# Kernel optimization log

Measured on AMD Instinct MI355X. Metric: run time of the kernel, lower is better.

## Reference

```python
import jax, jax.numpy as jnp
from jax import lax
import numpy as np

K = 3          # kernelsize
RX = RY = 3.0  # dilated_rates * kernelsize
BN_EPS = 1e-3  # keras BatchNormalization default


def setup_inputs() -> dict:
    key = jax.random.key(0)
    k1, k2, k3 = jax.random.split(key, 3)
    B, H, W, C, F = 8, 128, 128, 64, 64
    return {
        "fmap": jax.random.normal(k1, (B, H, W, C), jnp.float32),
        "y2": jax.random.normal(k2, (B, H, W, 8), jnp.float32),
        "conv_w": jax.random.normal(k3, (K, K, C, F), jnp.float32) * np.sqrt(2.0 / (K * K * C)),
        "gamma": jnp.ones((F,), jnp.float32),
        "beta": jnp.zeros((F,), jnp.float32),
        "moving_mean": jnp.zeros((F,), jnp.float32),
        "moving_var": jnp.ones((F,), jnp.float32),
    }


def reference(fmap, y2, conv_w, gamma, beta, moving_mean, moving_var):
    B, H, W, C = fmap.shape
    HW = H * W
    N = HW * K * K

    xs = jnp.clip(jnp.flip(jnp.sort(y2[..., 0:4], axis=-1), -1)[..., 0:2], 1.0, W - 1)  # [B,H,W,2]
    ys = jnp.clip(jnp.flip(jnp.sort(y2[..., 4:8], axis=-1), -1)[..., 0:2], 1.0, H - 1)
    w = jnp.sum(xs, axis=-1, keepdims=True)  # [B,H,W,1]
    h = jnp.sum(ys, axis=-1, keepdims=True)

    # base pixel grids flattened as in the TF code: row[i*W+j]=i, column[i*W+j]=j
    row = jnp.repeat(jnp.arange(H, dtype=jnp.float32), W).reshape(HW, 1)
    column = jnp.tile(jnp.arange(W, dtype=jnp.float32), H).reshape(HW, 1)

    wf = (w / RX).reshape(B, HW, 1)
    w0 = (w * 1e-10).reshape(B, HW, 1)
    x_samp = jnp.concatenate([column - 1.0 - wf, column + w0, column + 1.0 + wf], axis=-1)  # [B,HW,3]
    x_samp = jnp.tile(x_samp.reshape(-1, H, W, 1), (1, 1, 1, K))  # [3B,H,W,3] (same layout as TF)

    hf = (h / RY).reshape(B, HW, 1)
    h0 = (h * 1e-10).reshape(B, HW, 1)
    y_samp = jnp.concatenate([row - 1.0 - hf, row + h0, row + 1.0 + hf], axis=-1)
    y_samp = jnp.tile(y_samp.reshape(-1, H, W, 1), (1, 1, 1, K))  # [3B,H,W,3]

    x_left = jnp.clip(jnp.floor(x_samp), 0.0, W - 1)
    x_right = jnp.clip(jnp.ceil(x_samp), 0.0, W - 1)
    y_top = jnp.clip(jnp.floor(y_samp), 0.0, H - 1)
    y_bottom = jnp.clip(jnp.ceil(y_samp), 0.0, H - 1)

    def flat(a):  # -> [B, N, 1] (broadcast over C replaces TF's tile)
        return a.reshape(-1, N)[:, :, None]

    xr_x = flat(x_right - x_samp)
    xl_x = flat(x_samp - x_left)
    yt_y = flat(y_samp - y_top)
    yb_y = flat(y_bottom - y_samp)

    idx_lt = (y_top * W + x_left).reshape(-1, N).astype(jnp.int32)
    idx_rt = (y_top * W + x_right).reshape(-1, N).astype(jnp.int32)
    idx_lb = (y_bottom * W + x_left).reshape(-1, N).astype(jnp.int32)
    idx_rb = (y_bottom * W + x_right).reshape(-1, N).astype(jnp.int32)

    fmap2 = fmap.reshape(B, HW, C)
    gather = lambda idx: jnp.take_along_axis(fmap2, idx[:, :, None], axis=1)  # [B,N,C]

    f_lt, f_rt = gather(idx_lt), gather(idx_rt)
    f_lb, f_rb = gather(idx_lb), gather(idx_rb)

    f = (xr_x * f_lt + xl_x * f_lb) * yb_y + (xr_x * f_rt + xl_x * f_rb) * yt_y  # [B,N,C]
    f = f.reshape(-1, H * K, W * K, C)  # [B, 3H, 3W, C]

    out = lax.conv_general_dilated(
        f, conv_w, window_strides=(K, K), padding="VALID",
        dimension_numbers=("NHWC", "HWIO", "NHWC"))  # [B,H,W,F]

    out = (out - moving_mean) * (gamma / jnp.sqrt(moving_var + BN_EPS)) + beta
    return jax.nn.relu(out)
```

## Files before the change

kernel.cpp:

```cpp
#include <hip/hip_runtime.h>

typedef __bf16 bf16x8 __attribute__((ext_vector_type(8)));
typedef float f32x4 __attribute__((ext_vector_type(4)));

__device__ __forceinline__ unsigned short f2bf(float f) {
  __bf16 h = (__bf16)f;
  return __builtin_bit_cast(unsigned short, h);
}

__global__ __launch_bounds__(256) void prep_kernel(
    const float* __restrict__ conv_w, const float* __restrict__ gamma,
    const float* __restrict__ beta, const float* __restrict__ mean,
    const float* __restrict__ var, unsigned short* __restrict__ wsB,
    float* __restrict__ bias) {
  int idx = blockIdx.x * 256 + threadIdx.x;
  if (idx >= 12288) return;
  int di    = idx >> 12;
  int r     = idx & 4095;
  int jblk  = r >> 10;
  int r2    = r & 1023;
  int kstep = r2 >> 9;
  int r3    = r2 & 511;
  int lane  = r3 >> 3;
  int i     = r3 & 7;
  int c   = kstep * 32 + 4 * (lane >> 4) + (i & 3) + 16 * (i >> 2);
  int fch = jblk * 16 + (lane & 15);
  float s = gamma[fch] * rsqrtf(var[fch] + 1e-3f);
  float v = conv_w[((di * 3 + 0) * 64 + c) * 64 + fch]
          + conv_w[((di * 3 + 1) * 64 + c) * 64 + fch]
          + conv_w[((di * 3 + 2) * 64 + c) * 64 + fch];
  wsB[idx] = f2bf(v * s);
  if (idx < 64) bias[idx] = beta[idx] - mean[idx] * (gamma[idx] * rsqrtf(var[idx] + 1e-3f));
}

__global__ __launch_bounds__(256, 4) void main_kernel(
    const float* __restrict__ fmap, const float* __restrict__ y2,
    const uint4* __restrict__ wsBq, const float* __restrict__ biasg,
    float* __restrict__ out) {
  __shared__ int   s_idx[4][384];
  __shared__ float s_wt[4][384];
  __shared__ uint2 fsA[16][64][2];

  const int t    = threadIdx.x;
  const int lane = t & 63;
  const int wave = t >> 6;
  const int b  = blockIdx.x & 7;
  const int oi = blockIdx.x >> 3;
  const float* fmapb = fmap + (size_t)b * (128 * 128 * 64);

  for (int u = t; u < 384; u += 256) {
    int j = u / 3;
    int a = u - j * 3;
    const float4* yp = reinterpret_cast<const float4*>(
        y2 + ((size_t)(b * 128 + oi) * 128 + j) * 8);
    float4 xv = yp[0];
    float4 yv = yp[1];

    float hi01 = fmaxf(xv.x, xv.y), lo01 = fminf(xv.x, xv.y);
    float hi23 = fmaxf(xv.z, xv.w), lo23 = fminf(xv.z, xv.w);
    float top1 = fmaxf(hi01, hi23);
    float top2 = fmaxf(fminf(hi01, hi23), (hi01 >= hi23) ? lo01 : lo23);
    float w = fminf(fmaxf(top1, 1.f), 127.f) + fminf(fmaxf(top2, 1.f), 127.f);

    hi01 = fmaxf(yv.x, yv.y); lo01 = fminf(yv.x, yv.y);
    hi23 = fmaxf(yv.z, yv.w); lo23 = fminf(yv.z, yv.w);
    top1 = fmaxf(hi01, hi23);
    top2 = fmaxf(fminf(hi01, hi23), (hi01 >= hi23) ? lo01 : lo23);
    float h = fminf(fmaxf(top1, 1.f), 127.f) + fminf(fmaxf(top2, 1.f), 127.f);

    float x, yy;
    if (a == 0)      { x = ((float)j - 1.0f) - w / 3.0f;  yy = ((float)oi - 1.0f) - h / 3.0f; }
    else if (a == 1) { x = (float)j + w * 1e-10f;         yy = (float)oi + h * 1e-10f; }
    else             { x = ((float)j + 1.0f) + w / 3.0f;  yy = ((float)oi + 1.0f) + h / 3.0f; }

    float xl = fminf(fmaxf(floorf(x), 0.f), 127.f);
    float xr = fminf(fmaxf(ceilf(x),  0.f), 127.f);
    float yt = fminf(fmaxf(floorf(yy), 0.f), 127.f);
    float yb = fminf(fmaxf(ceilf(yy),  0.f), 127.f);
    int ixl = (int)xl, ixr = (int)xr, iyt = (int)yt, iyb = (int)yb;
    s_idx[0][u] = (iyt * 128 + ixl) * 64;
    s_idx[1][u] = (iyt * 128 + ixr) * 64;
    s_idx[2][u] = (iyb * 128 + ixl) * 64;
    s_idx[3][u] = (iyb * 128 + ixr) * 64;
    s_wt[0][u] = xr - x;
    s_wt[1][u] = x - xl;
    s_wt[2][u] = yy - yt;
    s_wt[3][u] = yb - yy;
  }
  __syncthreads();

  float bias4[4];
  #pragma unroll
  for (int j = 0; j < 4; ++j) bias4[j] = biasg[j * 16 + (lane & 15)];

  f32x4 acc[2][4];
  #pragma unroll
  for (int p = 0; p < 2; ++p)
    #pragma unroll
    for (int j = 0; j < 4; ++j)
      acc[p][j] = (f32x4){0.f, 0.f, 0.f, 0.f};

  for (int di = 0; di < 3; ++di) {
    bf16x8 Bf[8];
    #pragma unroll
    for (int jk = 0; jk < 8; ++jk)
      Bf[jk] = __builtin_bit_cast(bf16x8, wsBq[(di * 8 + jk) * 64 + lane]);

    #pragma unroll 2
    for (int r = 0; r < 8; ++r) {
      int task = t + 256 * r;
      int up = task >> 4;
      int cg = task & 15;
      int c0 = cg * 4;
      int u  = di * 128 + up;
      int i0 = s_idx[0][u], i1 = s_idx[1][u], i2 = s_idx[2][u], i3 = s_idx[3][u];
      float4 lt = *reinterpret_cast<const float4*>(fmapb + i0 + c0);
      float4 rt = *reinterpret_cast<const float4*>(fmapb + i1 + c0);
      float4 lb = *reinterpret_cast<const float4*>(fmapb + i2 + c0);
      float4 rb = *reinterpret_cast<const float4*>(fmapb + i3 + c0);
      float xr_x = s_wt[0][u], xl_x = s_wt[1][u];
      float yt_y = s_wt[2][u], yb_y = s_wt[3][u];
      float v0 = (xr_x * lt.x + xl_x * lb.x) * yb_y + (xr_x * rt.x + xl_x * rb.x) * yt_y;
      float v1 = (xr_x * lt.y + xl_x * lb.y) * yb_y + (xr_x * rt.y + xl_x * rb.y) * yt_y;
      float v2 = (xr_x * lt.z + xl_x * lb.z) * yb_y + (xr_x * rt.z + xl_x * rb.z) * yt_y;
      float v3 = (xr_x * lt.w + xl_x * lb.w) * yb_y + (xr_x * rt.w + xl_x * rb.w) * yt_y;
      uint2 q;
      q.x = (unsigned)f2bf(v0) | ((unsigned)f2bf(v1) << 16);
      q.y = (unsigned)f2bf(v2) | ((unsigned)f2bf(v3) << 16);
      int kstep = cg >> 3, g = cg & 3, h = (cg >> 2) & 1;
      fsA[(up >> 4) * 2 + kstep][(up & 15) + 16 * g][h] = q;
    }
    __syncthreads();

    #pragma unroll
    for (int kstep = 0; kstep < 2; ++kstep) {
      #pragma unroll
      for (int p = 0; p < 2; ++p) {
        int pxblk = wave * 2 + p;
        bf16x8 a = __builtin_bit_cast(bf16x8,
            *reinterpret_cast<const uint4*>(&fsA[pxblk * 2 + kstep][lane][0]));
        #pragma unroll
        for (int j = 0; j < 4; ++j)
          acc[p][j] = __builtin_amdgcn_mfma_f32_16x16x32_bf16(a, Bf[j * 2 + kstep],
                                                              acc[p][j], 0, 0, 0);
      }
    }
    __syncthreads();
  }

  float* outb = out + ((size_t)(b * 128 + oi) * 128) * 64;
  #pragma unroll
  for (int p = 0; p < 2; ++p) {
    int pxB = (wave * 2 + p) * 16 + (lane >> 4) * 4;
    #pragma unroll
    for (int j = 0; j < 4; ++j) {
      int fch = j * 16 + (lane & 15);
      #pragma unroll
      for (int reg = 0; reg < 4; ++reg) {
        float v = acc[p][j][reg] + bias4[j];
        outb[(size_t)(pxB + reg) * 64 + fch] = fmaxf(v, 0.f);
      }
    }
  }
}

extern "C" void kernel_launch(void* const* d_in, const int* in_sizes, int n_in,
                              void* d_out, int out_size, void* d_ws, size_t ws_size,
                              hipStream_t stream) {
  const float* fmap   = (const float*)d_in[0];
  const float* y2     = (const float*)d_in[1];
  const float* conv_w = (const float*)d_in[2];
  const float* gamma  = (const float*)d_in[3];
  const float* beta   = (const float*)d_in[4];
  const float* mean   = (const float*)d_in[5];
  const float* var    = (const float*)d_in[6];
  float* outp = (float*)d_out;

  unsigned short* wsB = (unsigned short*)d_ws;
  float* bias = (float*)((char*)d_ws + 24576);

  prep_kernel<<<48, 256, 0, stream>>>(conv_w, gamma, beta, mean, var, wsB, bias);
  main_kernel<<<1024, 256, 0, stream>>>(fmap, y2, (const uint4*)d_ws, bias, outp);
}
```

Before: 34.10 us.

## Skip gathers for zero-weight samples, swizzle LDS tile, fold bias into accumulator

During setup, each sample position is classified by whether its bilinear weights can contribute. Contributing positions are compacted into a per-tap list in shared memory using LDS atomics, and the rest are written as zeros without any fmap gather or arithmetic. The centre tap's float offsets usually round to exact integers, so most of its gathers can be skipped. The fsA tile is also XOR-swizzled to reduce LDS bank conflicts, and the bias now initialises the accumulators. In exchange this adds atomics, an extra barrier and a divergent branch, and it assumes zero weights always give zero output, which does not hold if the gathered values contain inf or NaN.

After: 30.86 us. -9.5%, faster.

```diff
diff --git a/kernel.cpp b/kernel.cpp
--- a/kernel.cpp
+++ b/kernel.cpp
@@ -40,6 +40,8 @@
   __shared__ int   s_idx[4][384];
   __shared__ float s_wt[4][384];
   __shared__ uint2 fsA[16][64][2];
+  __shared__ unsigned char lst[3][128];
+  __shared__ int cnt[3], zc[3];
 
   const int t    = threadIdx.x;
   const int lane = t & 63;
@@ -47,6 +49,10 @@
   const int b  = blockIdx.x & 7;
   const int oi = blockIdx.x >> 3;
   const float* fmapb = fmap + (size_t)b * (128 * 128 * 64);
+
+  if (t < 3) cnt[t] = 0;
+  else if (t < 6) zc[t - 3] = 0;
+  __syncthreads();
 
   for (int u = t; u < 384; u += 256) {
     int j = u / 3;
@@ -82,10 +88,17 @@
     s_idx[1][u] = (iyt * 128 + ixr) * 64;
     s_idx[2][u] = (iyb * 128 + ixl) * 64;
     s_idx[3][u] = (iyb * 128 + ixr) * 64;
-    s_wt[0][u] = xr - x;
-    s_wt[1][u] = x - xl;
-    s_wt[2][u] = yy - yt;
-    s_wt[3][u] = yb - yy;
+    float xr_x = xr - x, xl_x = x - xl, yt_y = yy - yt, yb_y = yb - yy;
+    s_wt[0][u] = xr_x;
+    s_wt[1][u] = xl_x;
+    s_wt[2][u] = yt_y;
+    s_wt[3][u] = yb_y;
+
+    bool need = ((xr_x != 0.f) || (xl_x != 0.f)) && ((yb_y != 0.f) || (yt_y != 0.f));
+    int di = u >> 7;
+    int up = u & 127;
+    int pos = need ? atomicAdd(&cnt[di], 1) : (127 - atomicAdd(&zc[di], 1));
+    lst[di][pos] = (unsigned char)up;
   }
   __syncthreads();
 
@@ -98,47 +111,56 @@
   for (int p = 0; p < 2; ++p)
     #pragma unroll
     for (int j = 0; j < 4; ++j)
-      acc[p][j] = (f32x4){0.f, 0.f, 0.f, 0.f};
+      acc[p][j] = (f32x4){bias4[j], bias4[j], bias4[j], bias4[j]};
 
   for (int di = 0; di < 3; ++di) {
     bf16x8 Bf[8];
     #pragma unroll
     for (int jk = 0; jk < 8; ++jk)
       Bf[jk] = __builtin_bit_cast(bf16x8, wsBq[(di * 8 + jk) * 64 + lane]);
+
+    const int nzc = cnt[di];
 
     #pragma unroll 2
     for (int r = 0; r < 8; ++r) {
       int task = t + 256 * r;
-      int up = task >> 4;
-      int cg = task & 15;
-      int c0 = cg * 4;
-      int u  = di * 128 + up;
-      int i0 = s_idx[0][u], i1 = s_idx[1][u], i2 = s_idx[2][u], i3 = s_idx[3][u];
-      float4 lt = *reinterpret_cast<const float4*>(fmapb + i0 + c0);
-      float4 rt = *reinterpret_cast<const float4*>(fmapb + i1 + c0);
-      float4 lb = *reinterpret_cast<const float4*>(fmapb + i2 + c0);
-      float4 rb = *reinterpret_cast<const float4*>(fmapb + i3 + c0);
-      float xr_x = s_wt[0][u], xl_x = s_wt[1][u];
-      float yt_y = s_wt[2][u], yb_y = s_wt[3][u];
-      float v0 = (xr_x * lt.x + xl_x * lb.x) * yb_y + (xr_x * rt.x + xl_x * rb.x) * yt_y;
-      float v1 = (xr_x * lt.y + xl_x * lb.y) * yb_y + (xr_x * rt.y + xl_x * rb.y) * yt_y;
-      float v2 = (xr_x * lt.z + xl_x * lb.z) * yb_y + (xr_x * rt.z + xl_x * rb.z) * yt_y;
-      float v3 = (xr_x * lt.w + xl_x * lb.w) * yb_y + (xr_x * rt.w + xl_x * rb.w) * yt_y;
-      uint2 q;
-      q.x = (unsigned)f2bf(v0) | ((unsigned)f2bf(v1) << 16);
-      q.y = (unsigned)f2bf(v2) | ((unsigned)f2bf(v3) << 16);
-      int kstep = cg >> 3, g = cg & 3, h = (cg >> 2) & 1;
-      fsA[(up >> 4) * 2 + kstep][(up & 15) + 16 * g][h] = q;
+      int gidx = task >> 4;
+      int cg   = task & 15;
+      int up   = lst[di][gidx];
+      int kstep = cg >> 3, g = cg & 3, hh = (cg >> 2) & 1;
+      int sA  = (up >> 4) * 2 + kstep;
+      int lA  = (up & 15) + 16 * g;
+      int lsw = lA ^ (2 * g);
+      uint2 q = make_uint2(0u, 0u);
+      if (gidx < nzc) {
+        int c0 = cg * 4;
+        int u  = di * 128 + up;
+        int i0 = s_idx[0][u], i1 = s_idx[1][u], i2 = s_idx[2][u], i3 = s_idx[3][u];
+        float4 lt = *reinterpret_cast<const float4*>(fmapb + i0 + c0);
+        float4 rt = *reinterpret_cast<const float4*>(fmapb + i1 + c0);
+        float4 lb = *reinterpret_cast<const float4*>(fmapb + i2 + c0);
+        float4 rb = *reinterpret_cast<const float4*>(fmapb + i3 + c0);
+        float xr_x = s_wt[0][u], xl_x = s_wt[1][u];
+        float yt_y = s_wt[2][u], yb_y = s_wt[3][u];
+        float v0 = (xr_x * lt.x + xl_x * lb.x) * yb_y + (xr_x * rt.x + xl_x * rb.x) * yt_y;
+        float v1 = (xr_x * lt.y + xl_x * lb.y) * yb_y + (xr_x * rt.y + xl_x * rb.y) * yt_y;
+        float v2 = (xr_x * lt.z + xl_x * lb.z) * yb_y + (xr_x * rt.z + xl_x * rb.z) * yt_y;
+        float v3 = (xr_x * lt.w + xl_x * lb.w) * yb_y + (xr_x * rt.w + xl_x * rb.w) * yt_y;
+        q.x = (unsigned)f2bf(v0) | ((unsigned)f2bf(v1) << 16);
+        q.y = (unsigned)f2bf(v2) | ((unsigned)f2bf(v3) << 16);
+      }
+      fsA[sA][lsw][hh] = q;
     }
     __syncthreads();
 
+    const int lsr = lane ^ (2 * (lane >> 4));
     #pragma unroll
     for (int kstep = 0; kstep < 2; ++kstep) {
       #pragma unroll
       for (int p = 0; p < 2; ++p) {
         int pxblk = wave * 2 + p;
         bf16x8 a = __builtin_bit_cast(bf16x8,
-            *reinterpret_cast<const uint4*>(&fsA[pxblk * 2 + kstep][lane][0]));
+            *reinterpret_cast<const uint4*>(&fsA[pxblk * 2 + kstep][lsr][0]));
         #pragma unroll
         for (int j = 0; j < 4; ++j)
           acc[p][j] = __builtin_amdgcn_mfma_f32_16x16x32_bf16(a, Bf[j * 2 + kstep],
@@ -157,8 +179,7 @@
       int fch = j * 16 + (lane & 15);
       #pragma unroll
       for (int reg = 0; reg < 4; ++reg) {
-        float v = acc[p][j][reg] + bias4[j];
-        outb[(size_t)(pxB + reg) * 64 + fch] = fmaxf(v, 0.f);
+        outb[(size_t)(pxB + reg) * 64 + fch] = fmaxf(acc[p][j][reg], 0.f);
       }
     }
   }
```

## Gather bilinear samples directly into MFMA A-fragments, drop LDS staging

Applied to the files above, without the earlier changes.

Each lane now loads and interpolates the fmap samples for exactly the A-fragment elements it feeds to the MFMA, instead of writing bf16 samples to shared memory and reading them back. This removes the fsA buffer and two block barriers per di iteration. It also skips the gathers when all bilinear weights are zero, and folds the bias into the accumulator initialisation. In exchange, each lane issues more scattered 16-byte loads, and the loads from one lane are split across two 16-float channel groups rather than staying contiguous.

Result: slower. 48.78 us (+43.0%).

```diff
diff --git a/kernel.cpp b/kernel.cpp
--- a/kernel.cpp
+++ b/kernel.cpp
@@ -39,7 +39,6 @@
     float* __restrict__ out) {
   __shared__ int   s_idx[4][384];
   __shared__ float s_wt[4][384];
-  __shared__ uint2 fsA[16][64][2];
 
   const int t    = threadIdx.x;
   const int lane = t & 63;
@@ -89,16 +88,19 @@
   }
   __syncthreads();
 
+  const int px15 = lane & 15;
+  const int cgrp = lane >> 4;
+
   float bias4[4];
   #pragma unroll
-  for (int j = 0; j < 4; ++j) bias4[j] = biasg[j * 16 + (lane & 15)];
+  for (int j = 0; j < 4; ++j) bias4[j] = biasg[j * 16 + px15];
 
   f32x4 acc[2][4];
   #pragma unroll
   for (int p = 0; p < 2; ++p)
     #pragma unroll
     for (int j = 0; j < 4; ++j)
-      acc[p][j] = (f32x4){0.f, 0.f, 0.f, 0.f};
+      acc[p][j] = (f32x4){bias4[j], bias4[j], bias4[j], bias4[j]};
 
   for (int di = 0; di < 3; ++di) {
     bf16x8 Bf[8];
@@ -106,46 +108,50 @@
     for (int jk = 0; jk < 8; ++jk)
       Bf[jk] = __builtin_bit_cast(bf16x8, wsBq[(di * 8 + jk) * 64 + lane]);
 
-    #pragma unroll 2
-    for (int r = 0; r < 8; ++r) {
-      int task = t + 256 * r;
-      int up = task >> 4;
-      int cg = task & 15;
-      int c0 = cg * 4;
-      int u  = di * 128 + up;
-      int i0 = s_idx[0][u], i1 = s_idx[1][u], i2 = s_idx[2][u], i3 = s_idx[3][u];
-      float4 lt = *reinterpret_cast<const float4*>(fmapb + i0 + c0);
-      float4 rt = *reinterpret_cast<const float4*>(fmapb + i1 + c0);
-      float4 lb = *reinterpret_cast<const float4*>(fmapb + i2 + c0);
-      float4 rb = *reinterpret_cast<const float4*>(fmapb + i3 + c0);
-      float xr_x = s_wt[0][u], xl_x = s_wt[1][u];
-      float yt_y = s_wt[2][u], yb_y = s_wt[3][u];
-      float v0 = (xr_x * lt.x + xl_x * lb.x) * yb_y + (xr_x * rt.x + xl_x * rb.x) * yt_y;
-      float v1 = (xr_x * lt.y + xl_x * lb.y) * yb_y + (xr_x * rt.y + xl_x * rb.y) * yt_y;
-      float v2 = (xr_x * lt.z + xl_x * lb.z) * yb_y + (xr_x * rt.z + xl_x * rb.z) * yt_y;
-      float v3 = (xr_x * lt.w + xl_x * lb.w) * yb_y + (xr_x * rt.w + xl_x * rb.w) * yt_y;
-      uint2 q;
-      q.x = (unsigned)f2bf(v0) | ((unsigned)f2bf(v1) << 16);
-      q.y = (unsigned)f2bf(v2) | ((unsigned)f2bf(v3) << 16);
-      int kstep = cg >> 3, g = cg & 3, h = (cg >> 2) & 1;
-      fsA[(up >> 4) * 2 + kstep][(up & 15) + 16 * g][h] = q;
-    }
-    __syncthreads();
+    #pragma unroll
+    for (int p = 0; p < 2; ++p) {
+      const int up = (wave * 2 + p) * 16 + px15;
+      const int u  = di * 128 + up;
+      const int i0 = s_idx[0][u], i1 = s_idx[1][u];
+      const int i2 = s_idx[2][u], i3 = s_idx[3][u];
+      const float xr_x = s_wt[0][u], xl_x = s_wt[1][u];
+      const float yt_y = s_wt[2][u], yb_y = s_wt[3][u];
+      const bool need = ((xr_x != 0.f) || (xl_x != 0.f)) &&
+                        ((yb_y != 0.f) || (yt_y != 0.f));
 
-    #pragma unroll
-    for (int kstep = 0; kstep < 2; ++kstep) {
       #pragma unroll
-      for (int p = 0; p < 2; ++p) {
-        int pxblk = wave * 2 + p;
-        bf16x8 a = __builtin_bit_cast(bf16x8,
-            *reinterpret_cast<const uint4*>(&fsA[pxblk * 2 + kstep][lane][0]));
+      for (int kstep = 0; kstep < 2; ++kstep) {
+        uint4 aq = make_uint4(0u, 0u, 0u, 0u);
+        if (need) {
+          const int c0 = 4 * cgrp + 32 * kstep;
+          float4 lt0 = *reinterpret_cast<const float4*>(fmapb + i0 + c0);
+          float4 rt0 = *reinterpret_cast<const float4*>(fmapb + i1 + c0);
+          float4 lb0 = *reinterpret_cast<const float4*>(fmapb + i2 + c0);
+          float4 rb0 = *reinterpret_cast<const float4*>(fmapb + i3 + c0);
+          float4 lt1 = *reinterpret_cast<const float4*>(fmapb + i0 + c0 + 16);
+          float4 rt1 = *reinterpret_cast<const float4*>(fmapb + i1 + c0 + 16);
+          float4 lb1 = *reinterpret_cast<const float4*>(fmapb + i2 + c0 + 16);
+          float4 rb1 = *reinterpret_cast<const float4*>(fmapb + i3 + c0 + 16);
+          float v0 = (xr_x * lt0.x + xl_x * lb0.x) * yb_y + (xr_x * rt0.x + xl_x * rb0.x) * yt_y;
+          float v1 = (xr_x * lt0.y + xl_x * lb0.y) * yb_y + (xr_x * rt0.y + xl_x * rb0.y) * yt_y;
+          float v2 = (xr_x * lt0.z + xl_x * lb0.z) * yb_y + (xr_x * rt0.z + xl_x * rb0.z) * yt_y;
+          float v3 = (xr_x * lt0.w + xl_x * lb0.w) * yb_y + (xr_x * rt0.w + xl_x * rb0.w) * yt_y;
+          float v4 = (xr_x * lt1.x + xl_x * lb1.x) * yb_y + (xr_x * rt1.x + xl_x * rb1.x) * yt_y;
+          float v5 = (xr_x * lt1.y + xl_x * lb1.y) * yb_y + (xr_x * rt1.y + xl_x * rb1.y) * yt_y;
+          float v6 = (xr_x * lt1.z + xl_x * lb1.z) * yb_y + (xr_x * rt1.z + xl_x * rb1.z) * yt_y;
+          float v7 = (xr_x * lt1.w + xl_x * lb1.w) * yb_y + (xr_x * rt1.w + xl_x * rb1.w) * yt_y;
+          aq.x = (unsigned)f2bf(v0) | ((unsigned)f2bf(v1) << 16);
+          aq.y = (unsigned)f2bf(v2) | ((unsigned)f2bf(v3) << 16);
+          aq.z = (unsigned)f2bf(v4) | ((unsigned)f2bf(v5) << 16);
+          aq.w = (unsigned)f2bf(v6) | ((unsigned)f2bf(v7) << 16);
+        }
+        bf16x8 a = __builtin_bit_cast(bf16x8, aq);
         #pragma unroll
         for (int j = 0; j < 4; ++j)
           acc[p][j] = __builtin_amdgcn_mfma_f32_16x16x32_bf16(a, Bf[j * 2 + kstep],
                                                               acc[p][j], 0, 0, 0);
       }
     }
-    __syncthreads();
   }
 
   float* outb = out + ((size_t)(b * 128 + oi) * 128) * 64;
@@ -154,11 +160,10 @@
     int pxB = (wave * 2 + p) * 16 + (lane >> 4) * 4;
     #pragma unroll
     for (int j = 0; j < 4; ++j) {
-      int fch = j * 16 + (lane & 15);
+      int fch = j * 16 + px15;
       #pragma unroll
       for (int reg = 0; reg < 4; ++reg) {
-        float v = acc[p][j][reg] + bias4[j];
-        outb[(size_t)(pxB + reg) * 64 + fch] = fmaxf(v, 0.f);
+        outb[(size_t)(pxB + reg) * 64 + fch] = fmaxf(acc[p][j][reg], 0.f);
       }
     }
   }
```

## Make each wave own its pixels to replace block barriers with wave barriers

Applied to the files above, without the earlier changes.

Each wave now computes its own sample indices and weights, gathers and stages only the pixels it later feeds to MFMA, and uses a per-wave LDS region. This lets the block-wide __syncthreads be replaced by wave barriers. The change also adds an XOR swizzle on the LDS layout to avoid bank conflicts, skips gathers when the bilinear weights are all zero, and folds the bias into the accumulator initialisation. Relying on wave barriers assumes LDS visibility within a wave, and the zero-weight branch can introduce divergence.

Measured after the change: 32.21 us. 5.5% less time.

```diff
diff --git a/kernel.cpp b/kernel.cpp
--- a/kernel.cpp
+++ b/kernel.cpp
@@ -39,7 +39,7 @@
     float* __restrict__ out) {
   __shared__ int   s_idx[4][384];
   __shared__ float s_wt[4][384];
-  __shared__ uint2 fsA[16][64][2];
+  __shared__ uint2 fsA[4][4][64][2];
 
   const int t    = threadIdx.x;
   const int lane = t & 63;
@@ -48,57 +48,73 @@
   const int oi = blockIdx.x >> 3;
   const float* fmapb = fmap + (size_t)b * (128 * 128 * 64);
 
-  for (int u = t; u < 384; u += 256) {
-    int j = u / 3;
-    int a = u - j * 3;
-    const float4* yp = reinterpret_cast<const float4*>(
-        y2 + ((size_t)(b * 128 + oi) * 128 + j) * 8);
-    float4 xv = yp[0];
-    float4 yv = yp[1];
-
-    float hi01 = fmaxf(xv.x, xv.y), lo01 = fminf(xv.x, xv.y);
-    float hi23 = fmaxf(xv.z, xv.w), lo23 = fminf(xv.z, xv.w);
-    float top1 = fmaxf(hi01, hi23);
-    float top2 = fmaxf(fminf(hi01, hi23), (hi01 >= hi23) ? lo01 : lo23);
-    float w = fminf(fmaxf(top1, 1.f), 127.f) + fminf(fmaxf(top2, 1.f), 127.f);
-
-    hi01 = fmaxf(yv.x, yv.y); lo01 = fminf(yv.x, yv.y);
-    hi23 = fmaxf(yv.z, yv.w); lo23 = fminf(yv.z, yv.w);
-    top1 = fmaxf(hi01, hi23);
-    top2 = fmaxf(fminf(hi01, hi23), (hi01 >= hi23) ? lo01 : lo23);
-    float h = fminf(fmaxf(top1, 1.f), 127.f) + fminf(fmaxf(top2, 1.f), 127.f);
-
-    float x, yy;
-    if (a == 0)      { x = ((float)j - 1.0f) - w / 3.0f;  yy = ((float)oi - 1.0f) - h / 3.0f; }
-    else if (a == 1) { x = (float)j + w * 1e-10f;         yy = (float)oi + h * 1e-10f; }
-    else             { x = ((float)j + 1.0f) + w / 3.0f;  yy = ((float)oi + 1.0f) + h / 3.0f; }
-
-    float xl = fminf(fmaxf(floorf(x), 0.f), 127.f);
-    float xr = fminf(fmaxf(ceilf(x),  0.f), 127.f);
-    float yt = fminf(fmaxf(floorf(yy), 0.f), 127.f);
-    float yb = fminf(fmaxf(ceilf(yy),  0.f), 127.f);
-    int ixl = (int)xl, ixr = (int)xr, iyt = (int)yt, iyb = (int)yb;
-    s_idx[0][u] = (iyt * 128 + ixl) * 64;
-    s_idx[1][u] = (iyt * 128 + ixr) * 64;
-    s_idx[2][u] = (iyb * 128 + ixl) * 64;
-    s_idx[3][u] = (iyb * 128 + ixr) * 64;
-    s_wt[0][u] = xr - x;
-    s_wt[1][u] = x - xl;
-    s_wt[2][u] = yy - yt;
-    s_wt[3][u] = yb - yy;
+  #pragma unroll
+  for (int it = 0; it < 2; ++it) {
+    int e = lane + 64 * it;
+    if (e < 96) {
+      int di  = e >> 5;
+      int upl = e & 31;
+      int up  = wave * 32 + upl;
+      int u   = di * 128 + up;
+      int j   = u / 3;
+      int a   = u - j * 3;
+      const float4* yp = reinterpret_cast<const float4*>(
+          y2 + ((size_t)(b * 128 + oi) * 128 + j) * 8);
+      float4 xv = yp[0];
+      float4 yv = yp[1];
+
+      float hi01 = fmaxf(xv.x, xv.y), lo01 = fminf(xv.x, xv.y);
+      float hi23 = fmaxf(xv.z, xv.w), lo23 = fminf(xv.z, xv.w);
+      float top1 = fmaxf(hi01, hi23);
+      float top2 = fmaxf(fminf(hi01, hi23), (hi01 >= hi23) ? lo01 : lo23);
+      float w = fminf(fmaxf(top1, 1.f), 127.f) + fminf(fmaxf(top2, 1.f), 127.f);
+
+      hi01 = fmaxf(yv.x, yv.y); lo01 = fminf(yv.x, yv.y);
+      hi23 = fmaxf(yv.z, yv.w); lo23 = fminf(yv.z, yv.w);
+      top1 = fmaxf(hi01, hi23);
+      top2 = fmaxf(fminf(hi01, hi23), (hi01 >= hi23) ? lo01 : lo23);
+      float h = fminf(fmaxf(top1, 1.f), 127.f) + fminf(fmaxf(top2, 1.f), 127.f);
+
+      float x, yy;
+      if (a == 0)      { x = ((float)j - 1.0f) - w / 3.0f;  yy = ((float)oi - 1.0f) - h / 3.0f; }
+      else if (a == 1) { x = (float)j + w * 1e-10f;         yy = (float)oi + h * 1e-10f; }
+      else             { x = ((float)j + 1.0f) + w / 3.0f;  yy = ((float)oi + 1.0f) + h / 3.0f; }
+
+      float xl = fminf(fmaxf(floorf(x), 0.f), 127.f);
+      float xr = fminf(fmaxf(ceilf(x),  0.f), 127.f);
+      float yt = fminf(fmaxf(floorf(yy), 0.f), 127.f);
+      float yb = fminf(fmaxf(ceilf(yy),  0.f), 127.f);
+      int ixl = (int)xl, ixr = (int)xr, iyt = (int)yt, iyb = (int)yb;
+      s_idx[0][u] = (iyt * 128 + ixl) * 64;
+      s_idx[1][u] = (iyt * 128 + ixr) * 64;
+      s_idx[2][u] = (iyb * 128 + ixl) * 64;
+      s_idx[3][u] = (iyb * 128 + ixr) * 64;
+      s_wt[0][u] = xr - x;
+      s_wt[1][u] = x - xl;
+      s_wt[2][u] = yy - yt;
+      s_wt[3][u] = yb - yy;
+    }
   }
-  __syncthreads();
-
+  __builtin_amdgcn_wave_barrier();
+
+  const int px15 = lane & 15;
   float bias4[4];
   #pragma unroll
-  for (int j = 0; j < 4; ++j) bias4[j] = biasg[j * 16 + (lane & 15)];
+  for (int j = 0; j < 4; ++j) bias4[j] = biasg[j * 16 + px15];
 
   f32x4 acc[2][4];
   #pragma unroll
   for (int p = 0; p < 2; ++p)
     #pragma unroll
     for (int j = 0; j < 4; ++j)
-      acc[p][j] = (f32x4){0.f, 0.f, 0.f, 0.f};
+      acc[p][j] = (f32x4){bias4[j], bias4[j], bias4[j], bias4[j]};
+
+  const int cg    = lane & 15;
+  const int g     = cg & 3;
+  const int hh    = (cg >> 2) & 1;
+  const int kstepS= cg >> 3;
+  const int upg   = lane >> 4;
+  const int lsr   = lane ^ (2 * (lane >> 4));
 
   for (int di = 0; di < 3; ++di) {
     bf16x8 Bf[8];
@@ -106,46 +122,49 @@
     for (int jk = 0; jk < 8; ++jk)
       Bf[jk] = __builtin_bit_cast(bf16x8, wsBq[(di * 8 + jk) * 64 + lane]);
 
-    #pragma unroll 2
+    #pragma unroll 4
     for (int r = 0; r < 8; ++r) {
-      int task = t + 256 * r;
-      int up = task >> 4;
-      int cg = task & 15;
-      int c0 = cg * 4;
-      int u  = di * 128 + up;
-      int i0 = s_idx[0][u], i1 = s_idx[1][u], i2 = s_idx[2][u], i3 = s_idx[3][u];
-      float4 lt = *reinterpret_cast<const float4*>(fmapb + i0 + c0);
-      float4 rt = *reinterpret_cast<const float4*>(fmapb + i1 + c0);
-      float4 lb = *reinterpret_cast<const float4*>(fmapb + i2 + c0);
-      float4 rb = *reinterpret_cast<const float4*>(fmapb + i3 + c0);
+      int upl = r * 4 + upg;
+      int up  = wave * 32 + upl;
+      int u   = di * 128 + up;
       float xr_x = s_wt[0][u], xl_x = s_wt[1][u];
       float yt_y = s_wt[2][u], yb_y = s_wt[3][u];
-      float v0 = (xr_x * lt.x + xl_x * lb.x) * yb_y + (xr_x * rt.x + xl_x * rb.x) * yt_y;
-      float v1 = (xr_x * lt.y + xl_x * lb.y) * yb_y + (xr_x * rt.y + xl_x * rb.y) * yt_y;
-      float v2 = (xr_x * lt.z + xl_x * lb.z) * yb_y + (xr_x * rt.z + xl_x * rb.z) * yt_y;
-      float v3 = (xr_x * lt.w + xl_x * lb.w) * yb_y + (xr_x * rt.w + xl_x * rb.w) * yt_y;
-      uint2 q;
-      q.x = (unsigned)f2bf(v0) | ((unsigned)f2bf(v1) << 16);
-      q.y = (unsigned)f2bf(v2) | ((unsigned)f2bf(v3) << 16);
-      int kstep = cg >> 3, g = cg & 3, h = (cg >> 2) & 1;
-      fsA[(up >> 4) * 2 + kstep][(up & 15) + 16 * g][h] = q;
-    }
-    __syncthreads();
+      bool need = ((xr_x != 0.f) || (xl_x != 0.f)) &&
+                  ((yb_y != 0.f) || (yt_y != 0.f));
+      uint2 q = make_uint2(0u, 0u);
+      if (need) {
+        int c0 = cg * 4;
+        int i0 = s_idx[0][u], i1 = s_idx[1][u];
+        int i2 = s_idx[2][u], i3 = s_idx[3][u];
+        float4 lt = *reinterpret_cast<const float4*>(fmapb + i0 + c0);
+        float4 rt = *reinterpret_cast<const float4*>(fmapb + i1 + c0);
+        float4 lb = *reinterpret_cast<const float4*>(fmapb + i2 + c0);
+        float4 rb = *reinterpret_cast<const float4*>(fmapb + i3 + c0);
+        float v0 = (xr_x * lt.x + xl_x * lb.x) * yb_y + (xr_x * rt.x + xl_x * rb.x) * yt_y;
+        float v1 = (xr_x * lt.y + xl_x * lb.y) * yb_y + (xr_x * rt.y + xl_x * rb.y) * yt_y;
+        float v2 = (xr_x * lt.z + xl_x * lb.z) * yb_y + (xr_x * rt.z + xl_x * rb.z) * yt_y;
+        float v3 = (xr_x * lt.w + xl_x * lb.w) * yb_y + (xr_x * rt.w + xl_x * rb.w) * yt_y;
+        q.x = (unsigned)f2bf(v0) | ((unsigned)f2bf(v1) << 16);
+        q.y = (unsigned)f2bf(v2) | ((unsigned)f2bf(v3) << 16);
+      }
+      int lpp = ((upl & 15) | (g << 4)) ^ (g << 1);
+      fsA[wave][(upl >> 4) * 2 + kstepS][lpp][hh] = q;
+    }
+    __builtin_amdgcn_wave_barrier();
 
     #pragma unroll
     for (int kstep = 0; kstep < 2; ++kstep) {
       #pragma unroll
       for (int p = 0; p < 2; ++p) {
-        int pxblk = wave * 2 + p;
         bf16x8 a = __builtin_bit_cast(bf16x8,
-            *reinterpret_cast<const uint4*>(&fsA[pxblk * 2 + kstep][lane][0]));
+            *reinterpret_cast<const uint4*>(&fsA[wave][p * 2 + kstep][lsr][0]));
         #pragma unroll
         for (int j = 0; j < 4; ++j)
           acc[p][j] = __builtin_amdgcn_mfma_f32_16x16x32_bf16(a, Bf[j * 2 + kstep],
                                                               acc[p][j], 0, 0, 0);
       }
     }
-    __syncthreads();
+    __builtin_amdgcn_wave_barrier();
   }
 
   float* outb = out + ((size_t)(b * 128 + oi) * 128) * 64;
@@ -154,11 +173,10 @@
     int pxB = (wave * 2 + p) * 16 + (lane >> 4) * 4;
     #pragma unroll
     for (int j = 0; j < 4; ++j) {
-      int fch = j * 16 + (lane & 15);
+      int fch = j * 16 + px15;
       #pragma unroll
       for (int reg = 0; reg < 4; ++reg) {
-        float v = acc[p][j][reg] + bias4[j];
-        outb[(size_t)(pxB + reg) * 64 + fch] = fmaxf(v, 0.f);
+        outb[(size_t)(pxB + reg) * 64 + fch] = fmaxf(acc[p][j][reg], 0.f);
       }
     }
   }
```
